# Kernel tuning notes

Measured on AMD Instinct MI355X. Metric: run time of the kernel, lower is better.

Reference implementation:

```python
import jax, jax.numpy as jnp
import numpy as np

B, N, X, Y, W1, W2, D = 2, 6, 8, 8, 8, 8, 128
H, DH = 4, 32
L = X * Y          # number of windows
QT = N * W1 * W2   # tokens per window
EPS = 1e-5


def _ln(x, g, b):
    m = x.mean(-1, keepdims=True)
    v = ((x - m) ** 2).mean(-1, keepdims=True)
    return (x - m) * jax.lax.rsqrt(v + EPS) * g + b


def _win(t):
    # b n x y w1 w2 d -> b (x y) (n w1 w2) d
    return t.transpose(0, 2, 3, 1, 4, 5, 6).reshape(B, L, QT, D)


def setup_inputs() -> dict:
    key = jax.random.key(0)
    ks = jax.random.split(key, 12)
    s = 0.02
    inp = {
        'q': jax.random.normal(ks[0], (B, N, X, Y, W1, W2, D), jnp.float32),
        'k': jax.random.normal(ks[1], (B, N, X, Y, W1, W2, D), jnp.float32),
        'v': jax.random.normal(ks[2], (B, N, X, Y, W1, W2, D), jnp.float32),
        'skip': jax.random.normal(ks[3], (B, X, Y, W1, W2, D), jnp.float32),
        'gq': jnp.ones((D,), jnp.float32), 'betq': jnp.zeros((D,), jnp.float32),
        'gk': jnp.ones((D,), jnp.float32), 'betk': jnp.zeros((D,), jnp.float32),
        'gv': jnp.ones((D,), jnp.float32), 'betv': jnp.zeros((D,), jnp.float32),
        'wq': jax.random.normal(ks[4], (D, H * DH), jnp.float32) * s,
        'bq': jnp.zeros((H * DH,), jnp.float32),
        'wk': jax.random.normal(ks[5], (D, H * DH), jnp.float32) * s,
        'bk': jnp.zeros((H * DH,), jnp.float32),
        'wv': jax.random.normal(ks[6], (D, H * DH), jnp.float32) * s,
        'bv': jnp.zeros((H * DH,), jnp.float32),
        'wp': jax.random.normal(ks[7], (H * DH, D), jnp.float32) * s,
        'bp': jnp.zeros((D,), jnp.float32),
    }
    return inp


def reference(q, k, v, skip, gq, betq, gk, betk, gv, betv,
              wq, bq, wk, bk, wv, bv, wp, bp):
    scale = DH ** -0.5
    qw, kw, vw = _win(q), _win(k), _win(v)
    # LayerNorm + Linear QKV, split heads: (b, l, T, h, dh)
    qh = (_ln(qw, gq, betq) @ wq + bq).reshape(B, L, QT, H, DH)
    kh = (_ln(kw, gk, betk) @ wk + bk).reshape(B, L, QT, H, DH)
    vh = (_ln(vw, gv, betv) @ wv + bv).reshape(B, L, QT, H, DH)
    dot = scale * jnp.einsum('blqhd,blkhd->bhlqk', qh, kh)
    att = jax.nn.softmax(dot, axis=-1)
    a = jnp.einsum('bhlqk,blkhd->blqhd', att, vh).reshape(B, L, QT, H * DH)
    # b (x y) (n w1 w2) d -> b n x y w1 w2 d
    a = a.reshape(B, X, Y, N, W1, W2, H * DH).transpose(0, 3, 1, 2, 4, 5, 6)
    z = a @ wp + bp
    z = z.mean(1)  # average over views
    return z + skip
```

## Files before the change

kernel.cpp:

```cpp
#include <hip/hip_runtime.h>


typedef unsigned short u16;
typedef __bf16 bf16x8 __attribute__((ext_vector_type(8)));
typedef __bf16 bf16x4 __attribute__((ext_vector_type(4)));
typedef float  f32x16 __attribute__((ext_vector_type(16)));
typedef unsigned short u16x8 __attribute__((ext_vector_type(8)));
typedef unsigned short u16x4 __attribute__((ext_vector_type(4)));

union U8 { u16x8 u; bf16x8 b; u16x4 h[2]; };

#if __has_builtin(__builtin_amdgcn_exp2f)
#define EXP2(x) __builtin_amdgcn_exp2f(x)
#else
#define EXP2(x) exp2f(x)
#endif

__device__ __forceinline__ f32x16 mfma_bf16(bf16x8 a, bf16x8 b, f32x16 c){
  return __builtin_amdgcn_mfma_f32_32x32x16_bf16(a, b, c, 0, 0, 0);
}


__global__ __launch_bounds__(512) void k_prep(
    const float* __restrict__ wq, const float* __restrict__ bq,
    const float* __restrict__ gq, const float* __restrict__ betq,
    const float* __restrict__ wk, const float* __restrict__ bk,
    const float* __restrict__ gk, const float* __restrict__ betk,
    const float* __restrict__ wv, const float* __restrict__ bv,
    const float* __restrict__ gv, const float* __restrict__ betv,
    const float* __restrict__ wp,
    u16* __restrict__ wqT, u16* __restrict__ wkT, u16* __restrict__ wvT, u16* __restrict__ wpT,
    float* __restrict__ bq2, float* __restrict__ bk2, float* __restrict__ bv2,
    float* __restrict__ uq2, float* __restrict__ uk2, float* __restrict__ uv2)
{
  __shared__ float wls[128*129];
  __shared__ float gls[128], bls[128];
  __shared__ float redb[512], redu[512];
  const float ALPHA_Q = 0.17677669529663687f * 1.4426950408889634f;
  int wsel = blockIdx.x, tid = threadIdx.x;
  const float *w, *bb, *g, *bet; u16* wT; float *b2, *u2; float alpha;
  if (wsel == 0){ w=wq; bb=bq; g=gq; bet=betq; wT=wqT; b2=bq2; u2=uq2; alpha=ALPHA_Q; }
  else if (wsel == 1){ w=wk; bb=bk; g=gk; bet=betk; wT=wkT; b2=bk2; u2=uk2; alpha=1.f; }
  else if (wsel == 2){ w=wv; bb=bv; g=gv; bet=betv; wT=wvT; b2=bv2; u2=uv2; alpha=1.f; }
  else { w=wp; bb=nullptr; g=nullptr; bet=nullptr; wT=wpT; b2=nullptr; u2=nullptr; alpha=1.f; }

  if (tid < 128){
    gls[tid] = g ? g[tid] : 1.f;
    bls[tid] = bet ? bet[tid] : 0.f;
  }
  const float4* w4 = (const float4*)w;
  #pragma unroll
  for (int i = 0; i < 8; i++){
    int idx = tid + i*512;
    int row = idx >> 5, c4 = (idx & 31) * 4;
    float4 x = w4[idx];
    wls[row*129 + c4 + 0] = x.x;
    wls[row*129 + c4 + 1] = x.y;
    wls[row*129 + c4 + 2] = x.z;
    wls[row*129 + c4 + 3] = x.w;
  }
  __syncthreads();
  int n = tid >> 2, qp = tid & 3;
  float sb = 0.f, su = 0.f;
  alignas(16) __bf16 tmp[32];
  #pragma unroll
  for (int kk = 0; kk < 32; kk++){
    int k2 = qp*32 + kk;
    float wv_ = wls[k2*129 + n];
    float gv_ = gls[k2];
    sb += bls[k2] * wv_;
    su += gv_ * wv_;
    tmp[kk] = (__bf16)(wv_ * gv_ * alpha);
  }
  #pragma unroll
  for (int j = 0; j < 4; j++)
    *(bf16x8*)(wT + n*128 + qp*32 + j*8) = *(bf16x8*)&tmp[j*8];
  redb[tid] = sb; redu[tid] = su;
  __syncthreads();
  if (qp == 0 && bb){
    float s = bb[n] + redb[tid] + redb[tid+1] + redb[tid+2] + redb[tid+3];
    float u = redu[tid] + redu[tid+1] + redu[tid+2] + redu[tid+3];
    b2[n] = s * alpha;
    u2[n] = u * alpha;
  }
}

__global__ __launch_bounds__(256) void k_lnproj(
    const float* __restrict__ qg, const float* __restrict__ kg, const float* __restrict__ vg,
    const u16* __restrict__ wqT, const u16* __restrict__ wkT, const u16* __restrict__ wvT,
    const float* __restrict__ bq2, const float* __restrict__ bk2, const float* __restrict__ bv2,
    const float* __restrict__ uq2, const float* __restrict__ uk2, const float* __restrict__ uv2,
    u16* __restrict__ qh, u16* __restrict__ kh, u16* __restrict__ vh)
{
  __shared__ alignas(16) u16 Abf[64*136];
  __shared__ float s1s[64], s2s[64];
  int bid = blockIdx.x, tid = threadIdx.x;
  int which = bid % 3;
  int t = bid / 3;
  int n = t % 6, bl = t / 6;
  const float* src; const u16* wT; const float *b2, *u2; u16* dstb;
  if (which == 0){ src=qg; wT=wqT; b2=bq2; u2=uq2; dstb=qh; }
  else if (which == 1){ src=kg; wT=wkT; b2=bk2; u2=uk2; dstb=kh; }
  else { src=vg; wT=wvT; b2=bv2; u2=uv2; dstb=vh; }
  int b = bl >> 6, l = bl & 63;
  const float4* s4 = (const float4*)(src + (size_t)((b*6 + n)*64 + l)*64*128);
  int row = tid >> 2, j = tid & 3;
  float s1 = 0.f, s2 = 0.f;
  #pragma unroll
  for (int i = 0; i < 8; i++){
    float4 xv = s4[row*32 + i*4 + j];
    s1 += xv.x + xv.y + xv.z + xv.w;
    s2 += xv.x*xv.x + xv.y*xv.y + xv.z*xv.z + xv.w*xv.w;
    bf16x4 pk;
    pk[0] = (__bf16)xv.x; pk[1] = (__bf16)xv.y;
    pk[2] = (__bf16)xv.z; pk[3] = (__bf16)xv.w;
    *(bf16x4*)&Abf[row*136 + (i*4 + j)*4] = pk;
  }
  s1 += __shfl_xor(s1, 1, 64); s1 += __shfl_xor(s1, 2, 64);
  s2 += __shfl_xor(s2, 1, 64); s2 += __shfl_xor(s2, 2, 64);
  if (j == 0){
    float m = s1 * (1.f/128.f);
    float r = rsqrtf(s2 * (1.f/128.f) - m*m + 1e-5f);
    s1s[row] = r;
    s2s[row] = r * m;
  }
  __syncthreads();
  int wave = tid >> 6, lane = tid & 63, lm = lane & 31, lh = lane >> 5;
  bf16x8 bfr[8];
  const u16* wrow = wT + (32*wave + lm)*128 + lh*8;
  #pragma unroll
  for (int ks = 0; ks < 8; ks++) bfr[ks] = *(const bf16x8*)(wrow + ks*16);
  f32x16 acc0, acc1;
  #pragma unroll
  for (int r = 0; r < 16; r++){ acc0[r]=0.f; acc1[r]=0.f; }
  #pragma unroll
  for (int ks = 0; ks < 8; ks++){
    bf16x8 a0 = *(const bf16x8*)&Abf[lm*136       + ks*16 + lh*8];
    bf16x8 a1 = *(const bf16x8*)&Abf[(32+lm)*136  + ks*16 + lh*8];
    acc0 = mfma_bf16(a0, bfr[ks], acc0);
    acc1 = mfma_bf16(a1, bfr[ks], acc1);
  }
  int col = 32*wave + lm;
  float u2c = u2[col], bc = b2[col];
  u16* dst = dstb + ((size_t)(bl*4 + wave)*384 + n*64)*32 + lm;
  #pragma unroll
  for (int r = 0; r < 16; r++){
    int row0 = (r&3) + 8*(r>>2) + 4*lh;
    float y0 = s1s[row0]     * acc0[r] - s2s[row0]     * u2c + bc;
    float y1 = s1s[row0+32]  * acc1[r] - s2s[row0+32]  * u2c + bc;
    *(__bf16*)&dst[(size_t)row0*32]      = (__bf16)y0;
    *(__bf16*)&dst[(size_t)(32+row0)*32] = (__bf16)y1;
  }
}

__global__ __launch_bounds__(384) void k_attn(
    const u16* __restrict__ qh, const u16* __restrict__ kh, const u16* __restrict__ vh,
    u16* __restrict__ abar)
{
  __shared__ alignas(16) u16 vts[32*392];
  __shared__ float abar_s[64*32];
  int bid = blockIdx.x, tid = threadIdx.x;
  int h = bid & 3, bl = bid >> 2;
  const u16* qb = qh + (size_t)bid * (384*32);
  const u16* kb = kh + (size_t)bid * (384*32);
  const u16* vb = vh + (size_t)bid * (384*32);

  int wave = tid >> 6, lane = tid & 63, lm = lane & 31, lh = lane >> 5;
  int n = wave;
  int rot = 2*n;

  const u16* qbase = qb + (size_t)(n*64 + lm)*32 + lh*8;
  bf16x8 qfA0 = *(const bf16x8*)(qbase);
  bf16x8 qfA1 = *(const bf16x8*)(qbase + 16);
  bf16x8 qfB0 = *(const bf16x8*)(qbase + 32*32);
  bf16x8 qfB1 = *(const bf16x8*)(qbase + 32*32 + 16);

  #pragma unroll
  for (int i = 0; i < 4; i++){
    int c = tid + i*384;
    int key = c >> 2, part = c & 3;
    int u = key & 31, tt = key >> 5;
    int a = u >> 2;
    int anew = (a & 4) | ((a & 1) << 1) | ((a >> 1) & 1);
    int pos = tt*32 + anew*4 + (u & 3);
    u16x8 vv = *(const u16x8*)(vb + key*32 + part*8);
    #pragma unroll
    for (int jj = 0; jj < 8; jj++) vts[(part*8 + jj)*392 + pos] = vv[jj];
  }
  for (int idx = tid; idx < 2048; idx += 384) abar_s[idx] = 0.f;
  __syncthreads();

  const u16* vrow = &vts[lm*392 + 8*lh];
  const u16* krow = kb + lm*32 + lh*8;

  bf16x8 ones;
  #pragma unroll
  for (int j = 0; j < 8; j++) ones[j] = (__bf16)1.0f;

  f32x16 oA, oB, slA, slB;
  #pragma unroll
  for (int r = 0; r < 16; r++){ oA[r]=0.f; oB[r]=0.f; slA[r]=0.f; slB[r]=0.f; }

  bf16x8 kf0 = *(const bf16x8*)(krow + rot*1024);
  bf16x8 kf1 = *(const bf16x8*)(krow + rot*1024 + 16);
  U8 v0, v1;
  v0.u = *(const u16x8*)(vrow + rot*32);
  v1.u = *(const u16x8*)(vrow + rot*32 + 16);

  #pragma unroll
  for (int kt = 0; kt < 12; kt++){
    bf16x8 nk0, nk1; U8 nv0, nv1;
    if (kt < 11){
      int te = kt + 1 + rot; if (te >= 12) te -= 12;
      nk0 = *(const bf16x8*)(krow + te*1024);
      nk1 = *(const bf16x8*)(krow + te*1024 + 16);
      nv0.u = *(const u16x8*)(vrow + te*32);
      nv1.u = *(const u16x8*)(vrow + te*32 + 16);
    }
    __builtin_amdgcn_sched_barrier(0);
    f32x16 sa, sb_;
    #pragma unroll
    for (int r = 0; r < 16; r++){ sa[r] = 0.f; sb_[r] = 0.f; }
    __builtin_amdgcn_s_setprio(1);
    sa  = mfma_bf16(kf0, qfA0, sa);
    sb_ = mfma_bf16(kf0, qfB0, sb_);
    sa  = mfma_bf16(kf1, qfA1, sa);
    sb_ = mfma_bf16(kf1, qfB1, sb_);
    __builtin_amdgcn_s_setprio(0);
    U8 pA0, pA1, pB0, pB1;
    #pragma unroll
    for (int r = 0; r < 8; r++){
      pA0.b[r] = (__bf16)EXP2(sa[r]);
      pA1.b[r] = (__bf16)EXP2(sa[r+8]);
      pB0.b[r] = (__bf16)EXP2(sb_[r]);
      pB1.b[r] = (__bf16)EXP2(sb_[r+8]);
    }
    __builtin_amdgcn_s_setprio(1);
    oA  = mfma_bf16(pA0.b, v0.b, oA);
    oB  = mfma_bf16(pB0.b, v0.b, oB);
    slA = mfma_bf16(pA0.b, ones, slA);
    slB = mfma_bf16(pB0.b, ones, slB);
    oA  = mfma_bf16(pA1.b, v1.b, oA);
    oB  = mfma_bf16(pB1.b, v1.b, oB);
    slA = mfma_bf16(pA1.b, ones, slA);
    slB = mfma_bf16(pB1.b, ones, slB);
    __builtin_amdgcn_s_setprio(0);
    if (kt < 11){ kf0 = nk0; kf1 = nk1; v0 = nv0; v1 = nv1; }
  }

  #pragma unroll
  for (int r = 0; r < 16; r++){
    int q_l = (r&3) + 8*(r>>2) + 4*lh;
    float ia = (1.f/6.f) * __builtin_amdgcn_rcpf(slA[r]);
    float ib = (1.f/6.f) * __builtin_amdgcn_rcpf(slB[r]);
    atomicAdd(&abar_s[q_l*32 + lm], oA[r]*ia);
    atomicAdd(&abar_s[(32 + q_l)*32 + lm], oB[r]*ib);
  }
  __syncthreads();
  u16* ob = abar + (size_t)(bl*64)*128 + h*32;
  for (int idx = tid; idx < 2048; idx += 384){
    int w12 = idx >> 5, dh = idx & 31;
    *(__bf16*)&ob[(size_t)w12*128 + dh] = (__bf16)abar_s[idx];
  }
}

__global__ __launch_bounds__(256) void k_out(
    const u16* __restrict__ abar, const u16* __restrict__ wpT,
    const float* __restrict__ bp, const float* __restrict__ skip,
    float* __restrict__ out)
{
  __shared__ alignas(16) u16 Als[64*136];
  int tid = threadIdx.x;
  int R0 = blockIdx.x * 64;
  #pragma unroll
  for (int i = 0; i < 4; i++){
    int c = tid + i*256;
    int row = c >> 4, part = c & 15;
    *(u16x8*)&Als[row*136 + part*8] = *(const u16x8*)(abar + (size_t)(R0+row)*128 + part*8);
  }
  __syncthreads();
  int wave = tid >> 6, lane = tid & 63, lm = lane & 31, lh = lane >> 5;
  bf16x8 bfr[8];
  const u16* wrow = wpT + (32*wave + lm)*128 + lh*8;
  #pragma unroll
  for (int ks = 0; ks < 8; ks++) bfr[ks] = *(const bf16x8*)(wrow + ks*16);
  f32x16 acc0, acc1;
  #pragma unroll
  for (int r = 0; r < 16; r++){ acc0[r]=0.f; acc1[r]=0.f; }
  #pragma unroll
  for (int ks = 0; ks < 8; ks++){
    bf16x8 a0 = *(const bf16x8*)&Als[lm*136      + ks*16 + lh*8];
    bf16x8 a1 = *(const bf16x8*)&Als[(32+lm)*136 + ks*16 + lh*8];
    acc0 = mfma_bf16(a0, bfr[ks], acc0);
    acc1 = mfma_bf16(a1, bfr[ks], acc1);
  }
  float bias = bp[32*wave + lm];
  #pragma unroll
  for (int r = 0; r < 16; r++){
    int row0 = (r&3) + 8*(r>>2) + 4*lh;
    size_t f0 = (size_t)(R0 + row0)*128 + 32*wave + lm;
    out[f0] = acc0[r] + bias + skip[f0];
    size_t f1 = (size_t)(R0 + 32 + row0)*128 + 32*wave + lm;
    out[f1] = acc1[r] + bias + skip[f1];
  }
}

extern "C" void kernel_launch(void* const* d_in, const int* in_sizes, int n_in,
                              void* d_out, int out_size, void* d_ws, size_t ws_size,
                              hipStream_t stream)
{
  const float* q    = (const float*)d_in[0];
  const float* k    = (const float*)d_in[1];
  const float* v    = (const float*)d_in[2];
  const float* skip = (const float*)d_in[3];
  const float* gq   = (const float*)d_in[4];
  const float* betq = (const float*)d_in[5];
  const float* gk   = (const float*)d_in[6];
  const float* betk = (const float*)d_in[7];
  const float* gv   = (const float*)d_in[8];
  const float* betv = (const float*)d_in[9];
  const float* wq   = (const float*)d_in[10];
  const float* bq   = (const float*)d_in[11];
  const float* wk   = (const float*)d_in[12];
  const float* bk   = (const float*)d_in[13];
  const float* wv   = (const float*)d_in[14];
  const float* bv   = (const float*)d_in[15];
  const float* wp   = (const float*)d_in[16];
  const float* bp   = (const float*)d_in[17];
  float* out = (float*)d_out;

  char* ws = (char*)d_ws;
  u16* wqT = (u16*)ws;
  u16* wkT = wqT + 16384;
  u16* wvT = wkT + 16384;
  u16* wpT = wvT + 16384;
  float* bq2 = (float*)(ws + 131072);
  float* bk2 = bq2 + 128;
  float* bv2 = bk2 + 128;
  float* uq2 = bv2 + 128;
  float* uk2 = uq2 + 128;
  float* uv2 = uk2 + 128;
  u16* qh = (u16*)(ws + 134144);
  u16* kh = qh + 6291456;
  u16* vh = kh + 6291456;
  u16* abar = vh + 6291456;

  k_prep  <<<4,    512, 0, stream>>>(wq,bq,gq,betq, wk,bk,gk,betk, wv,bv,gv,betv, wp,
                                     wqT,wkT,wvT,wpT, bq2,bk2,bv2, uq2,uk2,uv2);
  k_lnproj<<<2304, 256, 0, stream>>>(q,k,v, wqT,wkT,wvT, bq2,bk2,bv2, uq2,uk2,uv2, qh,kh,vh);
  k_attn  <<<512,  384, 0, stream>>>(qh,kh,vh, abar);
  k_out   <<<128,  256, 0, stream>>>(abar, wpT, bp, skip, out);
}
```

Before: 215.3 us.

## Split prep and output kernels across more blocks; simplify attention K/V loads

k_prep now spreads each weight matrix over 4 blocks of 32 output columns (16 blocks instead of 4). Only 128 of the 512 threads in each block do the transpose and reduction. k_out halves the rows per block to 32, giving 256 blocks, to fill more compute units. The attention loop drops its rotated, software-prefetched K/V register pipeline and loads each tile inside the loop, which removes the sched barrier but may expose load latency.

```diff
diff --git a/kernel.cpp b/kernel.cpp
--- a/kernel.cpp
+++ b/kernel.cpp
@@ -33,11 +33,12 @@
     float* __restrict__ bq2, float* __restrict__ bk2, float* __restrict__ bv2,
     float* __restrict__ uq2, float* __restrict__ uk2, float* __restrict__ uv2)
 {
-  __shared__ float wls[128*129];
+  __shared__ float wls[128*33];
   __shared__ float gls[128], bls[128];
-  __shared__ float redb[512], redu[512];
+  __shared__ float redb[128], redu[128];
   const float ALPHA_Q = 0.17677669529663687f * 1.4426950408889634f;
-  int wsel = blockIdx.x, tid = threadIdx.x;
+  int bid = blockIdx.x, tid = threadIdx.x;
+  int wsel = bid >> 2, chunk = bid & 3;
   const float *w, *bb, *g, *bet; u16* wT; float *b2, *u2; float alpha;
   if (wsel == 0){ w=wq; bb=bq; g=gq; bet=betq; wT=wqT; b2=bq2; u2=uq2; alpha=ALPHA_Q; }
   else if (wsel == 1){ w=wk; bb=bk; g=gk; bet=betk; wT=wkT; b2=bk2; u2=uk2; alpha=1.f; }
@@ -50,38 +51,45 @@
   }
   const float4* w4 = (const float4*)w;
   #pragma unroll
-  for (int i = 0; i < 8; i++){
+  for (int i = 0; i < 2; i++){
     int idx = tid + i*512;
-    int row = idx >> 5, c4 = (idx & 31) * 4;
-    float4 x = w4[idx];
-    wls[row*129 + c4 + 0] = x.x;
-    wls[row*129 + c4 + 1] = x.y;
-    wls[row*129 + c4 + 2] = x.z;
-    wls[row*129 + c4 + 3] = x.w;
-  }
-  __syncthreads();
-  int n = tid >> 2, qp = tid & 3;
-  float sb = 0.f, su = 0.f;
-  alignas(16) __bf16 tmp[32];
-  #pragma unroll
-  for (int kk = 0; kk < 32; kk++){
-    int k2 = qp*32 + kk;
-    float wv_ = wls[k2*129 + n];
-    float gv_ = gls[k2];
-    sb += bls[k2] * wv_;
-    su += gv_ * wv_;
-    tmp[kk] = (__bf16)(wv_ * gv_ * alpha);
-  }
-  #pragma unroll
-  for (int j = 0; j < 4; j++)
-    *(bf16x8*)(wT + n*128 + qp*32 + j*8) = *(bf16x8*)&tmp[j*8];
-  redb[tid] = sb; redu[tid] = su;
-  __syncthreads();
-  if (qp == 0 && bb){
-    float s = bb[n] + redb[tid] + redb[tid+1] + redb[tid+2] + redb[tid+3];
-    float u = redu[tid] + redu[tid+1] + redu[tid+2] + redu[tid+3];
-    b2[n] = s * alpha;
-    u2[n] = u * alpha;
+    int row = idx >> 3, f4c = idx & 7;
+    float4 x = w4[row*32 + chunk*8 + f4c];
+    wls[row*33 + f4c*4 + 0] = x.x;
+    wls[row*33 + f4c*4 + 1] = x.y;
+    wls[row*33 + f4c*4 + 2] = x.z;
+    wls[row*33 + f4c*4 + 3] = x.w;
+  }
+  __syncthreads();
+  if (tid < 128){
+    int nl = tid >> 2, qp = tid & 3;
+    float sb = 0.f, su = 0.f;
+    alignas(16) __bf16 tmp[32];
+    #pragma unroll
+    for (int kk = 0; kk < 32; kk++){
+      int k2 = qp*32 + kk;
+      float wv_ = wls[k2*33 + nl];
+      float gv_ = gls[k2];
+      sb += bls[k2] * wv_;
+      su += gv_ * wv_;
+      tmp[kk] = (__bf16)(wv_ * gv_ * alpha);
+    }
+    int n = chunk*32 + nl;
+    #pragma unroll
+    for (int j = 0; j < 4; j++)
+      *(bf16x8*)(wT + n*128 + qp*32 + j*8) = *(bf16x8*)&tmp[j*8];
+    redb[tid] = sb; redu[tid] = su;
+  }
+  __syncthreads();
+  if (tid < 128){
+    int nl = tid >> 2, qp = tid & 3;
+    if (qp == 0 && bb){
+      int n = chunk*32 + nl;
+      float s = bb[n] + redb[tid] + redb[tid+1] + redb[tid+2] + redb[tid+3];
+      float u = redu[tid] + redu[tid+1] + redu[tid+2] + redu[tid+3];
+      b2[n] = s * alpha;
+      u2[n] = u * alpha;
+    }
   }
 }
 
@@ -167,7 +175,6 @@
 
   int wave = tid >> 6, lane = tid & 63, lm = lane & 31, lh = lane >> 5;
   int n = wave;
-  int rot = 2*n;
 
   const u16* qbase = qb + (size_t)(n*64 + lm)*32 + lh*8;
   bf16x8 qfA0 = *(const bf16x8*)(qbase);
@@ -201,23 +208,10 @@
   #pragma unroll
   for (int r = 0; r < 16; r++){ oA[r]=0.f; oB[r]=0.f; slA[r]=0.f; slB[r]=0.f; }
 
-  bf16x8 kf0 = *(const bf16x8*)(krow + rot*1024);
-  bf16x8 kf1 = *(const bf16x8*)(krow + rot*1024 + 16);
-  U8 v0, v1;
-  v0.u = *(const u16x8*)(vrow + rot*32);
-  v1.u = *(const u16x8*)(vrow + rot*32 + 16);
-
   #pragma unroll
   for (int kt = 0; kt < 12; kt++){
-    bf16x8 nk0, nk1; U8 nv0, nv1;
-    if (kt < 11){
-      int te = kt + 1 + rot; if (te >= 12) te -= 12;
-      nk0 = *(const bf16x8*)(krow + te*1024);
-      nk1 = *(const bf16x8*)(krow + te*1024 + 16);
-      nv0.u = *(const u16x8*)(vrow + te*32);
-      nv1.u = *(const u16x8*)(vrow + te*32 + 16);
-    }
-    __builtin_amdgcn_sched_barrier(0);
+    bf16x8 kf0 = *(const bf16x8*)(krow + kt*1024);
+    bf16x8 kf1 = *(const bf16x8*)(krow + kt*1024 + 16);
     f32x16 sa, sb_;
     #pragma unroll
     for (int r = 0; r < 16; r++){ sa[r] = 0.f; sb_[r] = 0.f; }
@@ -227,6 +221,9 @@
     sa  = mfma_bf16(kf1, qfA1, sa);
     sb_ = mfma_bf16(kf1, qfB1, sb_);
     __builtin_amdgcn_s_setprio(0);
+    U8 v0, v1;
+    v0.u = *(const u16x8*)(vrow + kt*32);
+    v1.u = *(const u16x8*)(vrow + kt*32 + 16);
     U8 pA0, pA1, pB0, pB1;
     #pragma unroll
     for (int r = 0; r < 8; r++){
@@ -245,7 +242,6 @@
     slA = mfma_bf16(pA1.b, ones, slA);
     slB = mfma_bf16(pB1.b, ones, slB);
     __builtin_amdgcn_s_setprio(0);
-    if (kt < 11){ kf0 = nk0; kf1 = nk1; v0 = nv0; v1 = nv1; }
   }
 
   #pragma unroll
@@ -269,11 +265,11 @@
     const float* __restrict__ bp, const float* __restrict__ skip,
     float* __restrict__ out)
 {
-  __shared__ alignas(16) u16 Als[64*136];
+  __shared__ alignas(16) u16 Als[32*136];
   int tid = threadIdx.x;
-  int R0 = blockIdx.x * 64;
-  #pragma unroll
-  for (int i = 0; i < 4; i++){
+  int R0 = blockIdx.x * 32;
+  #pragma unroll
+  for (int i = 0; i < 2; i++){
     int c = tid + i*256;
     int row = c >> 4, part = c & 15;
     *(u16x8*)&Als[row*136 + part*8] = *(const u16x8*)(abar + (size_t)(R0+row)*128 + part*8);
@@ -284,24 +280,20 @@
   const u16* wrow = wpT + (32*wave + lm)*128 + lh*8;
   #pragma unroll
   for (int ks = 0; ks < 8; ks++) bfr[ks] = *(const bf16x8*)(wrow + ks*16);
-  f32x16 acc0, acc1;
-  #pragma unroll
-  for (int r = 0; r < 16; r++){ acc0[r]=0.f; acc1[r]=0.f; }
+  f32x16 acc;
+  #pragma unroll
+  for (int r = 0; r < 16; r++) acc[r] = 0.f;
   #pragma unroll
   for (int ks = 0; ks < 8; ks++){
-    bf16x8 a0 = *(const bf16x8*)&Als[lm*136      + ks*16 + lh*8];
-    bf16x8 a1 = *(const bf16x8*)&Als[(32+lm)*136 + ks*16 + lh*8];
-    acc0 = mfma_bf16(a0, bfr[ks], acc0);
-    acc1 = mfma_bf16(a1, bfr[ks], acc1);
+    bf16x8 a0 = *(const bf16x8*)&Als[lm*136 + ks*16 + lh*8];
+    acc = mfma_bf16(a0, bfr[ks], acc);
   }
   float bias = bp[32*wave + lm];
   #pragma unroll
   for (int r = 0; r < 16; r++){
     int row0 = (r&3) + 8*(r>>2) + 4*lh;
     size_t f0 = (size_t)(R0 + row0)*128 + 32*wave + lm;
-    out[f0] = acc0[r] + bias + skip[f0];
-    size_t f1 = (size_t)(R0 + 32 + row0)*128 + 32*wave + lm;
-    out[f1] = acc1[r] + bias + skip[f1];
+    out[f0] = acc[r] + bias + skip[f0];
   }
 }
 
@@ -345,9 +337,9 @@
   u16* vh = kh + 6291456;
   u16* abar = vh + 6291456;
 
-  k_prep  <<<4,    512, 0, stream>>>(wq,bq,gq,betq, wk,bk,gk,betk, wv,bv,gv,betv, wp,
+  k_prep  <<<16,   512, 0, stream>>>(wq,bq,gq,betq, wk,bk,gk,betk, wv,bv,gv,betv, wp,
                                      wqT,wkT,wvT,wpT, bq2,bk2,bv2, uq2,uk2,uv2);
   k_lnproj<<<2304, 256, 0, stream>>>(q,k,v, wqT,wkT,wvT, bq2,bk2,bv2, uq2,uk2,uv2, qh,kh,vh);
   k_attn  <<<512,  384, 0, stream>>>(qh,kh,vh, abar);
-  k_out   <<<128,  256, 0, stream>>>(abar, wpT, bp, skip, out);
-}
+  k_out   <<<256,  256, 0, stream>>>(abar, wpT, bp, skip, out);
+}
```

Result: faster. 205.9 us (-4.4%).
